# Kernel optimization log

Measured on AMD Instinct MI355X. Metric: run time of the kernel, lower is better.

## Reference

```python
import jax, jax.numpy as jnp
import numpy as np


def _build_idx():
    # Gather indices replicating the 36 overlapping 3x3 window slices.
    # Board layout: flat index = x*48 + y*6 + f  (8x8 squares, 6 features).
    idx = np.zeros((36, 54), dtype=np.int32)
    for i in range(36):
        x, y = i // 6, i % 6
        c = 0
        for ox in range(3):
            for oy in range(3):
                base = (x + ox) * 48 + (y + oy) * 6
                for f in range(6):
                    idx[i, c] = base + f
                    c += 1
    return jnp.asarray(idx)

IDX = _build_idx()  # [36, 54]
B = 65536


def setup_inputs() -> dict:
    key = jax.random.key(0)
    ks = jax.random.split(key, 13)
    rn = lambda k, shape, s=0.3: jax.random.normal(k, shape, dtype=jnp.float32) * s
    return {
        "inp": jax.random.normal(ks[0], (B, 385), dtype=jnp.float32),
        "W1": rn(ks[1], (16, 54)), "b1": rn(ks[2], (16,)),
        "W2": rn(ks[3], (16, 16)), "b2": rn(ks[4], (16,)),
        "W3": rn(ks[5], (2, 16)),  "b3": rn(ks[6], (2,)),
        "E1": rn(ks[7], (34, 73)), "e1": rn(ks[8], (34,)),
        "E2": rn(ks[9], (34, 34)), "e2": rn(ks[10], (34,)),
        "E3": rn(ks[11], (1, 34)), "e3": rn(ks[12], (1,)),
    }


def reference(inp, W1, b1, W2, b2, W3, b3, E1, e1, E2, e2, E3, e3):
    crelu = lambda x: jnp.clip(x, -1.0, 1.0)
    # One gather replaces 36 * 9 slice/cat ops: [B, 36, 54]
    w = inp[:, IDX]
    # Sight MLP applied to all 36 windows at once (torch Linear: x @ W.T + b)
    h = crelu(jnp.einsum('bws,os->bwo', w, W1) + b1)   # [B, 36, 16]
    h = crelu(jnp.einsum('bwi,oi->bwo', h, W2) + b2)   # [B, 36, 16]
    v = crelu(jnp.einsum('bwi,oi->bwo', h, W3) + b3)   # [B, 36, 2]
    # vision[i*2], vision[i*2+1] interleave == reshape of [36, 2]; append inp[384]
    vision = jnp.concatenate([v.reshape(v.shape[0], 72), inp[:, 384:385]], axis=-1)  # [B, 73]
    h = crelu(vision @ E1.T + e1)
    h = crelu(h @ E2.T + e2)
    return crelu(h @ E3.T + e3)  # [B, 1]
```

## Files before the change

kernel.cpp:

```cpp
#include <hip/hip_runtime.h>
#include <hip/hip_fp16.h>

typedef _Float16 half8v __attribute__((ext_vector_type(8)));
typedef __fp16  pk16x2 __attribute__((ext_vector_type(2)));
typedef float f32x4 __attribute__((ext_vector_type(4)));

#define DEV __device__ __forceinline__
DEV float crelu(float x) { return fminf(fmaxf(x, -1.0f), 1.0f); }

DEV unsigned int pkrtz_u32(float a, float b) {
    pk16x2 p = __builtin_amdgcn_cvt_pkrtz(a, b);
    return __builtin_bit_cast(unsigned int, p);
}

DEV void lgkm0() { asm volatile("s_waitcnt lgkmcnt(0)" ::: "memory"); }
DEV void cfence() { asm volatile("" ::: "memory"); }

__global__ void prep_kernel(const float* __restrict__ W1, const float* __restrict__ W2,
                            const float* __restrict__ W3, const float* __restrict__ E1,
                            const float* __restrict__ E2, const float* __restrict__ e1b,
                            const float* __restrict__ e2b, const float* __restrict__ E3,
                            float* __restrict__ ws) {
    int t = threadIdx.x + blockIdx.x * blockDim.x;
    if (t < 864) {
        int s = t >> 4, o = t & 15;
        ws[t] = W1[o * 54 + s];
    } else if (t < 864 + 256) {
        int u = t - 864; int i = u >> 4, o = u & 15;
        ws[t] = W2[o * 16 + i];
    } else if (t < 1120 + 32) {
        int u = t - 1120; int i = u >> 1, o = u & 1;
        ws[t] = W3[o * 16 + i];
    } else if (t >= 8192 && t < 8192 + 1536) {
        _Float16* fr = (_Float16*)((char*)ws + 19200);
        int u = t - 8192;
        int ks = u >> 9, l = (u >> 3) & 63, j = u & 7;
        int n = l & 15;
        int kg = ks * 32 + ((l >> 4) << 3) + j;
        int ox = kg / 24, rem = kg - ox * 24, cy = rem >> 3, f = rem & 7;
        float v = (kg < 72 && f < 6) ? W1[n * 54 + ox * 18 + cy * 6 + f] : 0.0f;
        fr[u] = (_Float16)v;
    } else if (t >= 10240 && t < 10240 + 512) {
        _Float16* fr = (_Float16*)((char*)ws + 19200) + 1536;
        int u = t - 10240;
        int l = u >> 3, j = u & 7;
        int n = l & 15;
        int k = ((l >> 4) << 3) + j;
        float v = (k < 16) ? W2[n * 16 + k] : 0.0f;
        fr[u] = (_Float16)v;
    } else if (t >= 12288 && t < 12288 + 4608) {
        _Float16* fr = (_Float16*)((char*)ws + 32768);
        int u = t - 12288;
        int ks = u / 1536, rem = u % 1536;
        int nt = rem / 512;
        int l = (rem >> 3) & 63, j = u & 7;
        int k = ks * 32 + ((l >> 4) << 3) + j;
        int o = nt * 16 + (l & 15);
        float v = (k < 73 && o < 34) ? E1[o * 73 + k] : 0.0f;
        fr[u] = (_Float16)v;
    } else if (t >= 18432 && t < 18432 + 3072) {
        _Float16* fr = (_Float16*)((char*)ws + 45056);
        int u = t - 18432;
        int ks = u / 1536, rem = u % 1536;
        int nt = rem / 512;
        int l = (rem >> 3) & 63, j = u & 7;
        int k = ks * 32 + ((l >> 4) << 3) + j;
        int o = nt * 16 + (l & 15);
        float v = (k < 34 && o < 34) ? E2[o * 34 + k] : 0.0f;
        fr[u] = (_Float16)v;
    } else if (t >= 22528 && t < 22528 + 48) {
        int u = t - 22528; ws[6000 + u] = (u < 34) ? e1b[u] : 0.0f;
    } else if (t >= 22592 && t < 22592 + 48) {
        int u = t - 22592; ws[6048 + u] = (u < 34) ? e2b[u] : 0.0f;
    } else if (t >= 22656 && t < 22656 + 48) {
        int u = t - 22656; ws[6096 + u] = (u < 34) ? E3[u] : 0.0f;
    }
}

__global__ __launch_bounds__(256, 2) void lila_kernel(
    const float* __restrict__ inp,
    const float* __restrict__ b1, const float* __restrict__ b2,
    const float* __restrict__ b3, const float* __restrict__ e3v,
    const float* __restrict__ ws, const _Float16* __restrict__ frag,
    float* __restrict__ out)
{
    __shared__ half8v lds[4 * 580];
    const int tid  = threadIdx.x;
    const int wid  = tid >> 6;
    const int lane = tid & 63;
    const int baseE = blockIdx.x * 16;
    const int baseP = baseE + wid * 4;

    half8v* grid = lds + wid * 580;
    half8v* h1   = grid + 288;
    _Float16* h1h = (_Float16*)h1;
    unsigned int* vloc = (unsigned int*)lds;
    _Float16* hset = (_Float16*)((char*)lds + 9280);

    const int r = lane & 15;
    const int g = lane >> 4;

    {
        const uint4 z = {0u, 0u, 0u, 0u};
        #pragma unroll
        for (int i = 0; i < 10; ++i) {
            const int idx = lane + i * 64;
            if (i < 9 || idx < 580)
                *reinterpret_cast<uint4*>(grid + idx) = z;
        }
    }
    cfence();

    {
        const int es = lane >> 4, m = lane & 15;
        const float* __restrict__ src = inp + (size_t)(baseP + es) * 385 + 24 * m;
        #pragma unroll
        for (int c = 0; c < 4; ++c) {
            float f0 = src[c * 6 + 0], f1 = src[c * 6 + 1], f2 = src[c * 6 + 2];
            float f3 = src[c * 6 + 3], f4 = src[c * 6 + 4], f5 = src[c * 6 + 5];
            uint4 q;
            q.x = pkrtz_u32(f0, f1);
            q.y = pkrtz_u32(f2, f3);
            q.z = pkrtz_u32(f4, f5);
            q.w = q.z;
            *reinterpret_cast<uint4*>(grid + es * 72 + 4 * m + c) = q;
        }
    }
    cfence();

    {
        const half8v* __restrict__ fr8 = (const half8v*)frag;
        half8v B1_0 = fr8[0 * 64 + lane];
        half8v B1_1 = fr8[1 * 64 + lane];
        half8v B1_2 = fr8[2 * 64 + lane];
        half8v B2f  = fr8[3 * 64 + lane];

        int off[3];
        #pragma unroll
        for (int ks = 0; ks < 3; ++ks) {
            int c = ks * 4 + g;
            int ox = c / 3, cy = c - 3 * ox;
            off[ks] = ox * 8 + cy;
        }

        const float bias1 = b1[r];
        const float bias2 = b2[r];

        int w = r, ebase = 0;
        #pragma unroll
        for (int t = 0; t < 9; ++t) {
            const int x = (w * 43) >> 8;
            const int y = w - x * 6;
            const int cellb = ebase + x * 8 + y;

            half8v a0 = grid[cellb + off[0]];
            half8v a1 = grid[cellb + off[1]];
            half8v a2 = grid[cellb + off[2]];

            f32x4 acc = {bias1, bias1, bias1, bias1};
            acc = __builtin_amdgcn_mfma_f32_16x16x32_f16(a0, B1_0, acc, 0, 0, 0);
            acc = __builtin_amdgcn_mfma_f32_16x16x32_f16(a1, B1_1, acc, 0, 0, 0);
            acc = __builtin_amdgcn_mfma_f32_16x16x32_f16(a2, B1_2, acc, 0, 0, 0);

            #pragma unroll
            for (int q = 0; q < 4; ++q)
                h1h[(t * 16 + g * 4 + q) * 16 + r] = (_Float16)crelu(acc[q]);
            cfence();

            half8v af = h1[(t * 16 + r) * 2 + g];
            f32x4 c2 = {bias2, bias2, bias2, bias2};
            c2 = __builtin_amdgcn_mfma_f32_16x16x32_f16(af, B2f, c2, 0, 0, 0);

            #pragma unroll
            for (int q = 0; q < 4; ++q)
                h1h[(t * 16 + g * 4 + q) * 16 + r] = (_Float16)crelu(c2[q]);

            w += 16;
            if (w >= 36) { w -= 36; ebase += 72; }
        }
    }

    __syncthreads();

    {
        const float* __restrict__ w3t = ws + 1120;
        const float b30 = b3[0], b31 = b3[1];
        #pragma unroll
        for (int rep = 0; rep < 3; ++rep) {
            const int wg = lane + rep * 64;
            if (rep < 2 || lane < 16) {
                half8v ha = h1[wg * 2 + 0];
                half8v hb = h1[wg * 2 + 1];
                float v0 = b30, v1 = b31;
                #pragma unroll
                for (int i = 0; i < 8; ++i) {
                    const float hv = (float)ha[i];
                    v0 = fmaf(hv, w3t[i * 2 + 0], v0);
                    v1 = fmaf(hv, w3t[i * 2 + 1], v1);
                }
                #pragma unroll
                for (int i = 0; i < 8; ++i) {
                    const float hv = (float)hb[i];
                    v0 = fmaf(hv, w3t[(8 + i) * 2 + 0], v0);
                    v1 = fmaf(hv, w3t[(8 + i) * 2 + 1], v1);
                }
                vloc[wid * 144 + wg] = pkrtz_u32(crelu(v0), crelu(v1));
            }
        }
    }

    __syncthreads();
    if (wid != 0) return;

    {
        const uint4 z = {0u, 0u, 0u, 0u};
        if (lane < 51) {
            *reinterpret_cast<uint4*>(hset + lane * 8) = z;
            *reinterpret_cast<uint4*>(hset + (lane + 51) * 8) = z;
        }
    }
    lgkm0();

    const half8v* __restrict__ e1f8 = (const half8v*)((const char*)ws + 32768);
    const half8v* __restrict__ e2f8 = (const half8v*)((const char*)ws + 45056);

    float biasA[3], bias2A[3], e3w[3];
    #pragma unroll
    for (int nt = 0; nt < 3; ++nt) {
        biasA[nt]  = ws[6000 + nt * 16 + r];
        bias2A[nt] = ws[6048 + nt * 16 + r];
        e3w[nt]    = ws[6096 + nt * 16 + r];
    }

    const uint4* vp4 = (const uint4*)(vloc + r * 36);
    const float xl = inp[(size_t)(baseE + r) * 385 + 384];

    f32x4 acc[3] = {{biasA[0], biasA[0], biasA[0], biasA[0]},
                    {biasA[1], biasA[1], biasA[1], biasA[1]},
                    {biasA[2], biasA[2], biasA[2], biasA[2]}};
    #pragma unroll
    for (int ks = 0; ks < 3; ++ks) {
        uint4 aw;
        if (ks < 2) {
            aw = vp4[ks * 4 + g];
        } else {
            if (g == 0)      aw = vp4[8];
            else if (g == 1) { aw.x = pkrtz_u32(xl, 0.0f); aw.y = 0u; aw.z = 0u; aw.w = 0u; }
            else             { aw.x = 0u; aw.y = 0u; aw.z = 0u; aw.w = 0u; }
        }
        const half8v af = __builtin_bit_cast(half8v, aw);
        #pragma unroll
        for (int nt = 0; nt < 3; ++nt)
            acc[nt] = __builtin_amdgcn_mfma_f32_16x16x32_f16(
                af, e1f8[(ks * 3 + nt) * 64 + lane], acc[nt], 0, 0, 0);
    }

    #pragma unroll
    for (int nt = 0; nt < 3; ++nt)
        #pragma unroll
        for (int q = 0; q < 4; ++q)
            hset[(g * 4 + q) * 48 + nt * 16 + r] = (_Float16)crelu(acc[nt][q]);
    lgkm0();

    f32x4 acc2[3] = {{bias2A[0], bias2A[0], bias2A[0], bias2A[0]},
                     {bias2A[1], bias2A[1], bias2A[1], bias2A[1]},
                     {bias2A[2], bias2A[2], bias2A[2], bias2A[2]}};
    #pragma unroll
    for (int ks = 0; ks < 2; ++ks) {
        const half8v af = *reinterpret_cast<const half8v*>(
            &hset[r * 48 + ks * 32 + g * 8]);
        #pragma unroll
        for (int nt = 0; nt < 3; ++nt)
            acc2[nt] = __builtin_amdgcn_mfma_f32_16x16x32_f16(
                af, e2f8[(ks * 3 + nt) * 64 + lane], acc2[nt], 0, 0, 0);
    }

    const float e3b = e3v[0];
    float s[4];
    #pragma unroll
    for (int q = 0; q < 4; ++q) {
        float part = crelu(acc2[0][q]) * e3w[0]
                   + crelu(acc2[1][q]) * e3w[1]
                   + crelu(acc2[2][q]) * e3w[2];
        part += __shfl_xor(part, 1);
        part += __shfl_xor(part, 2);
        part += __shfl_xor(part, 4);
        part += __shfl_xor(part, 8);
        s[q] = crelu(part + e3b);
    }
    if (r == 0) {
        float4 o4 = {s[0], s[1], s[2], s[3]};
        *reinterpret_cast<float4*>(out + baseE + g * 4) = o4;
    }
}

extern "C" void kernel_launch(void* const* d_in, const int* in_sizes, int n_in,
                              void* d_out, int out_size, void* d_ws, size_t ws_size,
                              hipStream_t stream) {
    const float* inp = (const float*)d_in[0];
    const float* W1  = (const float*)d_in[1];
    const float* b1  = (const float*)d_in[2];
    const float* W2  = (const float*)d_in[3];
    const float* b2  = (const float*)d_in[4];
    const float* W3  = (const float*)d_in[5];
    const float* b3  = (const float*)d_in[6];
    const float* E1  = (const float*)d_in[7];
    const float* e1  = (const float*)d_in[8];
    const float* E2  = (const float*)d_in[9];
    const float* e2  = (const float*)d_in[10];
    const float* E3  = (const float*)d_in[11];
    const float* e3  = (const float*)d_in[12];
    float* out = (float*)d_out;
    float* ws  = (float*)d_ws;
    const _Float16* frag = (const _Float16*)((const char*)d_ws + 19200);

    prep_kernel<<<89, 256, 0, stream>>>(W1, W2, W3, E1, E2, e1, e2, E3, ws);

    const int B = 65536;
    lila_kernel<<<B / 16, 256, 0, stream>>>(inp, b1, b2, b3, e3, ws, frag, out);
}
```

Measured before the change: 42.66 us.

## Keep sight MLP activations in registers via transposed MFMA and lane shuffles

Swaps the MFMA operand order so layer-1 outputs come out transposed, then passes them to the layer-2 MFMA with cross-lane shuffles instead of an LDS round trip. Layer 3 (16->2) is folded into the same loop with per-lane partial dot products and xor-shuffle reductions, which removes the separate pass over stored h1 and one __syncthreads. LDS use shrinks because the h1 buffers are gone, which may allow more blocks per CU. In exchange the loop does more shuffles and redundant per-lane work, and the weight fragment layout in the workspace must match the new operand order.

Result: faster. 39.22 us, median of 2 (-8.1%).

```diff
diff --git a/kernel.cpp b/kernel.cpp
--- a/kernel.cpp
+++ b/kernel.cpp
@@ -84,18 +84,16 @@
     const float* __restrict__ ws, const _Float16* __restrict__ frag,
     float* __restrict__ out)
 {
-    __shared__ half8v lds[4 * 580];
+    __shared__ half8v grids[4 * 288];
+    __shared__ unsigned int vloc[576];
+    __shared__ _Float16 hset[17 * 48];
     const int tid  = threadIdx.x;
     const int wid  = tid >> 6;
     const int lane = tid & 63;
     const int baseE = blockIdx.x * 16;
     const int baseP = baseE + wid * 4;
 
-    half8v* grid = lds + wid * 580;
-    half8v* h1   = grid + 288;
-    _Float16* h1h = (_Float16*)h1;
-    unsigned int* vloc = (unsigned int*)lds;
-    _Float16* hset = (_Float16*)((char*)lds + 9280);
+    half8v* grid = grids + wid * 288;
 
     const int r = lane & 15;
     const int g = lane >> 4;
@@ -103,9 +101,9 @@
     {
         const uint4 z = {0u, 0u, 0u, 0u};
         #pragma unroll
-        for (int i = 0; i < 10; ++i) {
+        for (int i = 0; i < 5; ++i) {
             const int idx = lane + i * 64;
-            if (i < 9 || idx < 580)
+            if (i < 4 || idx < 288)
                 *reinterpret_cast<uint4*>(grid + idx) = z;
         }
     }
@@ -130,10 +128,10 @@
 
     {
         const half8v* __restrict__ fr8 = (const half8v*)frag;
-        half8v B1_0 = fr8[0 * 64 + lane];
-        half8v B1_1 = fr8[1 * 64 + lane];
-        half8v B1_2 = fr8[2 * 64 + lane];
-        half8v B2f  = fr8[3 * 64 + lane];
+        half8v W1f0 = fr8[0 * 64 + lane];
+        half8v W1f1 = fr8[1 * 64 + lane];
+        half8v W1f2 = fr8[2 * 64 + lane];
+        half8v W2fA = fr8[3 * 64 + lane];
 
         int off[3];
         #pragma unroll
@@ -143,8 +141,19 @@
             off[ks] = ox * 8 + cy;
         }
 
-        const float bias1 = b1[r];
-        const float bias2 = b2[r];
+        float b1q[4], b2q[4], w3a[4], w3b[4];
+        const float* __restrict__ w3t = ws + 1120;
+        #pragma unroll
+        for (int q = 0; q < 4; ++q) {
+            b1q[q] = b1[g * 4 + q];
+            b2q[q] = b2[g * 4 + q];
+            w3a[q] = w3t[(g * 4 + q) * 2 + 0];
+            w3b[q] = w3t[(g * 4 + q) * 2 + 1];
+        }
+        const float b30 = b3[0], b31 = b3[1];
+
+        const int s0 = r + (((g << 1) + 0) & 3) * 16;
+        const int s1 = r + (((g << 1) + 1) & 3) * 16;
 
         int w = r, ebase = 0;
         #pragma unroll
@@ -157,55 +166,41 @@
             half8v a1 = grid[cellb + off[1]];
             half8v a2 = grid[cellb + off[2]];
 
-            f32x4 acc = {bias1, bias1, bias1, bias1};
-            acc = __builtin_amdgcn_mfma_f32_16x16x32_f16(a0, B1_0, acc, 0, 0, 0);
-            acc = __builtin_amdgcn_mfma_f32_16x16x32_f16(a1, B1_1, acc, 0, 0, 0);
-            acc = __builtin_amdgcn_mfma_f32_16x16x32_f16(a2, B1_2, acc, 0, 0, 0);
-
+            f32x4 acc = {b1q[0], b1q[1], b1q[2], b1q[3]};
+            acc = __builtin_amdgcn_mfma_f32_16x16x32_f16(W1f0, a0, acc, 0, 0, 0);
+            acc = __builtin_amdgcn_mfma_f32_16x16x32_f16(W1f1, a1, acc, 0, 0, 0);
+            acc = __builtin_amdgcn_mfma_f32_16x16x32_f16(W1f2, a2, acc, 0, 0, 0);
+
+            const unsigned int d0 = pkrtz_u32(crelu(acc[0]), crelu(acc[1]));
+            const unsigned int d1 = pkrtz_u32(crelu(acc[2]), crelu(acc[3]));
+            uint4 bw;
+            bw.x = (unsigned int)__shfl((int)d0, s0);
+            bw.y = (unsigned int)__shfl((int)d1, s0);
+            bw.z = (unsigned int)__shfl((int)d0, s1);
+            bw.w = (unsigned int)__shfl((int)d1, s1);
+            if (g >= 2) { bw.x = 0u; bw.y = 0u; bw.z = 0u; bw.w = 0u; }
+            const half8v B2in = __builtin_bit_cast(half8v, bw);
+
+            f32x4 c2 = {b2q[0], b2q[1], b2q[2], b2q[3]};
+            c2 = __builtin_amdgcn_mfma_f32_16x16x32_f16(W2fA, B2in, c2, 0, 0, 0);
+
+            float v0p = 0.0f, v1p = 0.0f;
             #pragma unroll
-            for (int q = 0; q < 4; ++q)
-                h1h[(t * 16 + g * 4 + q) * 16 + r] = (_Float16)crelu(acc[q]);
-            cfence();
-
-            half8v af = h1[(t * 16 + r) * 2 + g];
-            f32x4 c2 = {bias2, bias2, bias2, bias2};
-            c2 = __builtin_amdgcn_mfma_f32_16x16x32_f16(af, B2f, c2, 0, 0, 0);
-
-            #pragma unroll
-            for (int q = 0; q < 4; ++q)
-                h1h[(t * 16 + g * 4 + q) * 16 + r] = (_Float16)crelu(c2[q]);
+            for (int q = 0; q < 4; ++q) {
+                const float hv = crelu(c2[q]);
+                v0p = fmaf(hv, w3a[q], v0p);
+                v1p = fmaf(hv, w3b[q], v1p);
+            }
+            v0p += __shfl_xor(v0p, 16);
+            v0p += __shfl_xor(v0p, 32);
+            v1p += __shfl_xor(v1p, 16);
+            v1p += __shfl_xor(v1p, 32);
+            if (g == 0)
+                vloc[wid * 144 + (ebase >> 1) + w] =
+                    pkrtz_u32(crelu(v0p + b30), crelu(v1p + b31));
 
             w += 16;
             if (w >= 36) { w -= 36; ebase += 72; }
-        }
-    }
-
-    __syncthreads();
-
-    {
-        const float* __restrict__ w3t = ws + 1120;
-        const float b30 = b3[0], b31 = b3[1];
-        #pragma unroll
-        for (int rep = 0; rep < 3; ++rep) {
-            const int wg = lane + rep * 64;
-            if (rep < 2 || lane < 16) {
-                half8v ha = h1[wg * 2 + 0];
-                half8v hb = h1[wg * 2 + 1];
-                float v0 = b30, v1 = b31;
-                #pragma unroll
-                for (int i = 0; i < 8; ++i) {
-                    const float hv = (float)ha[i];
-                    v0 = fmaf(hv, w3t[i * 2 + 0], v0);
-                    v1 = fmaf(hv, w3t[i * 2 + 1], v1);
-                }
-                #pragma unroll
-                for (int i = 0; i < 8; ++i) {
-                    const float hv = (float)hb[i];
-                    v0 = fmaf(hv, w3t[(8 + i) * 2 + 0], v0);
-                    v1 = fmaf(hv, w3t[(8 + i) * 2 + 1], v1);
-                }
-                vloc[wid * 144 + wg] = pkrtz_u32(crelu(v0), crelu(v1));
-            }
         }
     }
 
```
